# Optimization experiments

Measured on AMD Instinct MI355X. Metric: run time of the kernel, lower is better.

The kernel has to match this reference:

```python
import jax, jax.numpy as jnp
import numpy as np

FDIM, HDIM, DIM = 512, 512, 256
B, N = 64, 4096


def setup_inputs() -> dict:
    key = jax.random.key(0)
    k1, k2, k3, k4, k5 = jax.random.split(key, 5)
    image_features = jax.random.normal(k1, (B, N, FDIM), dtype=jnp.float32)
    hidden_state = jax.random.normal(k2, (B, HDIM), dtype=jnp.float32)
    # nn.Linear weights: stored [out, in]; y = x @ W.T
    W_img = jax.random.normal(k3, (DIM, FDIM), dtype=jnp.float32) * (FDIM ** -0.5)
    W_hid = jax.random.normal(k4, (DIM, HDIM), dtype=jnp.float32) * (HDIM ** -0.5)
    W_score = jax.random.normal(k5, (1, DIM), dtype=jnp.float32) * (DIM ** -0.5)
    return {"image_features": image_features, "hidden_state": hidden_state,
            "W_img": W_img, "W_hid": W_hid, "W_score": W_score}


def reference(image_features, hidden_state, W_img, W_hid, W_score):
    # proj_image: [B, N, D]
    proj_image = jnp.einsum('bnf,df->bnd', image_features, W_img)
    # proj_hidden: [B, 1, D]
    proj_hidden = jnp.einsum('bh,dh->bd', hidden_state, W_hid)[:, None, :]
    combined = jnp.tanh(proj_image + proj_hidden)            # [B, N, D]
    scores = jnp.einsum('bnd,d->bn', combined, W_score[0])   # [B, N]
    weights = jax.nn.softmax(scores, axis=-1)                # [B, N]
    context = jnp.einsum('bn,bnf->bf', weights, image_features)  # [B, F]
    return (context, weights)
```

## Files before the change

### kernel.cpp

```cpp
#include <hip/hip_runtime.h>
#include <hip/hip_bf16.h>

#define B_ 64
#define N_ 4096
#define F_ 512
#define D_ 256
#define BM 32
#define APAD 520
#define NCHUNK (N_ / BM)
#define NBLK (B_ * NCHUNK)

typedef __attribute__((ext_vector_type(8))) short short8;
typedef __attribute__((ext_vector_type(4))) float f32x4;

__device__ __forceinline__ unsigned short f2bf(float f) {
  unsigned int u = __float_as_uint(f);
  u += 0x7FFFu + ((u >> 16) & 1u);
  return (unsigned short)(u >> 16);
}

__device__ __forceinline__ unsigned int pk2bf(float x, float y) {
  float2 f; f.x = x; f.y = y;
  __hip_bfloat162 h = __float22bfloat162_rn(f);
  union { __hip_bfloat162 h2; unsigned int u; } cv; cv.h2 = h;
  return cv.u;
}

__device__ __forceinline__ float fast_tanh(float x) {
  float e = __expf(-2.0f * fabsf(x));
  float t = (1.0f - e) / (1.0f + e);
  return copysignf(t, x);
}

#define SBAR                                                                   \
  do {                                                                         \
    __builtin_amdgcn_sched_barrier(0);                                         \
    __builtin_amdgcn_s_barrier();                                              \
    __builtin_amdgcn_sched_barrier(0);                                         \
  } while (0)

#define LGKM0                                                                  \
  do {                                                                         \
    asm volatile("s_waitcnt lgkmcnt(0)" ::: "memory");                         \
    __builtin_amdgcn_sched_barrier(0);                                         \
  } while (0)

__global__ void prep_w_kernel(const float* __restrict__ Wimg,
                              unsigned short* __restrict__ wfrag) {
  int d = blockIdx.x;
  int f = threadIdx.x;
  int q = f >> 5, lg = (f >> 3) & 3, e = f & 7;
  int lr = d & 15, d16 = d >> 4;
  int lane = lg * 16 + lr;
  int idx = ((q * 16 + d16) * 64 + lane) * 8 + e;
  wfrag[idx] = f2bf(Wimg[d * F_ + f]);
}

__global__ void prep_ph_kernel(const float* __restrict__ hid,
                               const float* __restrict__ Whid,
                               float* __restrict__ ph) {
  int b = blockIdx.x, d = threadIdx.x;
  const float4* hv = (const float4*)(hid + b * F_);
  const float4* wv = (const float4*)(Whid + d * F_);
  float acc = 0.f;
#pragma unroll 4
  for (int i = 0; i < 128; i++) {
    float4 h = hv[i], w = wv[i];
    acc += h.x * w.x + h.y * w.y + h.z * w.z + h.w * w.w;
  }
  ph[b * D_ + d] = acc;
}

__global__ __launch_bounds__(256, 4) void fused_kernel(
    const float* __restrict__ feat, const unsigned short* __restrict__ wfrag,
    const float* __restrict__ ph, const float* __restrict__ wscore,
    float* __restrict__ expw, float2* __restrict__ meta,
    float* __restrict__ part) {
  __shared__ unsigned short Afull[BM * APAD];
  __shared__ float red[BM][4];
  __shared__ float sbuf[BM];
  __shared__ float ewf[BM];

  int tid = threadIdx.x;
  int lane = tid & 63, wn = tid >> 6;
  int lr = lane & 15, lg = lane >> 4;

  int blk = blockIdx.x;
  int b = blk >> 7, chunk = blk & 127;
  int n0 = chunk * BM;

  const float* arow = feat + (size_t)(b * N_ + n0) * F_;

  f32x4 acc[2][4];
#pragma unroll
  for (int m = 0; m < 2; m++)
#pragma unroll
    for (int n = 0; n < 4; n++) acc[m][n] = (f32x4)0.f;

  int r2_[4], c4_[4];
#pragma unroll
  for (int i = 0; i < 4; i++) {
    int idx4 = tid + i * 256;
    r2_[i] = idx4 >> 5;
    c4_[i] = idx4 & 31;
  }

  float4 ra0[4], ra1[4];

#define LOADA(buf, p_)                                                         \
  _Pragma("unroll") for (int i = 0; i < 4; i++)                                \
      buf[i] = *(const float4*)(arow + (size_t)r2_[i] * F_ + (p_)*128 + c4_[i] * 4);

#define CVT(buf, p_)                                                           \
  _Pragma("unroll") for (int i = 0; i < 4; i++) {                              \
    unsigned int p0 = pk2bf(buf[i].x, buf[i].y);                               \
    unsigned int p1 = pk2bf(buf[i].z, buf[i].w);                               \
    *(uint2*)(Afull + r2_[i] * APAD + (p_)*128 + c4_[i] * 4) = make_uint2(p0, p1); \
  }

  const unsigned short* bbase = wfrag + (size_t)((wn * 4) * 64 + lane) * 8;

#define QSTEP(q_)                                                              \
  {                                                                            \
    short8 bf[4];                                                              \
    _Pragma("unroll") for (int n = 0; n < 4; n++)                              \
        bf[n] = *(const short8*)(bbase + (size_t)(((q_)*16 + n) * 64) * 8);    \
    short8 a0 = *(const short8*)(Afull + lr * APAD + (q_)*32 + lg * 8);        \
    short8 a1 = *(const short8*)(Afull + (16 + lr) * APAD + (q_)*32 + lg * 8); \
    _Pragma("unroll") for (int n = 0; n < 4; n++) {                            \
      acc[0][n] = __builtin_amdgcn_mfma_f32_16x16x32_bf16(a0, bf[n], acc[0][n], 0, 0, 0); \
      acc[1][n] = __builtin_amdgcn_mfma_f32_16x16x32_bf16(a1, bf[n], acc[1][n], 0, 0, 0); \
    }                                                                          \
  }

#define PHASE(p_) { QSTEP((p_)*4+0); QSTEP((p_)*4+1); QSTEP((p_)*4+2); QSTEP((p_)*4+3); }

  LOADA(ra0, 0);
  LOADA(ra1, 1);
  CVT(ra0, 0);
  LGKM0;
  SBAR;
  LOADA(ra0, 2);
  PHASE(0);
  CVT(ra1, 1);
  LGKM0;
  SBAR;
  LOADA(ra1, 3);
  PHASE(1);
  CVT(ra0, 2);
  LGKM0;
  SBAR;
  PHASE(2);
  CVT(ra1, 3);
  LGKM0;
  SBAR;
  PHASE(3);

  float ph4[4], wv4[4];
#pragma unroll
  for (int n = 0; n < 4; n++) {
    int d = wn * 64 + n * 16 + lr;
    ph4[n] = ph[b * D_ + d];
    wv4[n] = wscore[d];
  }
#pragma unroll
  for (int m = 0; m < 2; m++) {
#pragma unroll
    for (int j = 0; j < 4; j++) {
      float p = 0.f;
#pragma unroll
      for (int n = 0; n < 4; n++)
        p += fast_tanh(acc[m][n][j] + ph4[n]) * wv4[n];
      p += __shfl_xor(p, 1);
      p += __shfl_xor(p, 2);
      p += __shfl_xor(p, 4);
      p += __shfl_xor(p, 8);
      if (lr == 0) red[m * 16 + lg * 4 + j][wn] = p;
    }
  }
  __syncthreads();
  if (tid < BM) sbuf[tid] = red[tid][0] + red[tid][1] + red[tid][2] + red[tid][3];
  __syncthreads();

  float mb = -1e30f;
#pragma unroll
  for (int r = 0; r < BM; r++) mb = fmaxf(mb, sbuf[r]);
  if (tid < BM) {
    float e = __expf(sbuf[tid] - mb);
    ewf[tid] = e;
    expw[b * N_ + n0 + tid] = e;
    float l = e;
#pragma unroll
    for (int o = 1; o < 32; o <<= 1) l += __shfl_xor(l, o);
    if (tid == 0) meta[blk] = make_float2(mb, l);
  }
  __syncthreads();

  int f0 = tid * 2;
  float a0 = 0.f, a1 = 0.f;
#pragma unroll 8
  for (int r = 0; r < BM; r++) {
    float w = ewf[r];
    unsigned int v = *(const unsigned int*)(Afull + r * APAD + f0);
    a0 += w * __uint_as_float(v << 16);
    a1 += w * __uint_as_float(v & 0xffff0000u);
  }
  float2 o; o.x = a0; o.y = a1;
  *(float2*)(part + (size_t)blk * F_ + f0) = o;
}

__global__ void finalize_kernel(const float* __restrict__ part,
                                const float2* __restrict__ meta,
                                const float* __restrict__ expw,
                                float* __restrict__ ctx,
                                float* __restrict__ wout) {
  __shared__ float sm[NCHUNK], sl[NCHUNK], se[NCHUNK];
  int b = blockIdx.x, t = threadIdx.x;
  if (t < NCHUNK) {
    float2 ml = meta[b * NCHUNK + t];
    sm[t] = ml.x;
    sl[t] = ml.y;
  }
  __syncthreads();
  float M = -1e30f;
#pragma unroll 8
  for (int i = 0; i < NCHUNK; i++) M = fmaxf(M, sm[i]);
  float Z = 0.f;
#pragma unroll 8
  for (int i = 0; i < NCHUNK; i++) Z += sl[i] * __expf(sm[i] - M);
  if (t < NCHUNK) se[t] = __expf(sm[t] - M);
  __syncthreads();
  float invZ = 1.0f / Z;
  float acc = 0.f;
#pragma unroll 8
  for (int i = 0; i < NCHUNK; i++) acc += part[(size_t)(b * NCHUNK + i) * F_ + t] * se[i];
  ctx[b * F_ + t] = acc * invZ;
#pragma unroll
  for (int k = 0; k < 8; k++) {
    int n = k * 512 + t;
    wout[b * N_ + n] = expw[b * N_ + n] * se[n >> 5] * invZ;
  }
}

extern "C" void kernel_launch(void* const* d_in, const int* in_sizes, int n_in,
                              void* d_out, int out_size, void* d_ws, size_t ws_size,
                              hipStream_t stream) {
  const float* feat   = (const float*)d_in[0];
  const float* hid    = (const float*)d_in[1];
  const float* Wimg   = (const float*)d_in[2];
  const float* Whid   = (const float*)d_in[3];
  const float* Wscore = (const float*)d_in[4];

  float* ctx  = (float*)d_out;
  float* wout = (float*)d_out + B_ * F_;

  unsigned short* wfrag = (unsigned short*)d_ws;
  float*  ph    = (float*)((char*)d_ws + 262144);
  float*  expw  = (float*)((char*)d_ws + 327680);
  float2* meta  = (float2*)((char*)d_ws + 1376256);
  float*  part  = (float*)((char*)d_ws + 1441792);

  prep_w_kernel<<<D_, F_, 0, stream>>>(Wimg, wfrag);
  prep_ph_kernel<<<B_, D_, 0, stream>>>(hid, Whid, ph);
  fused_kernel<<<NBLK, 256, 0, stream>>>(feat, wfrag, ph, Wscore, expw, meta, part);
  finalize_kernel<<<B_, 512, 0, stream>>>(part, meta, expw, ctx, wout);
}
```

Baseline: 214.2 us.

## Load whole A tile up front with row-wise coalescing, then run MFMA loop

```diff
diff --git a/kernel.cpp b/kernel.cpp
--- a/kernel.cpp
+++ b/kernel.cpp
@@ -31,19 +31,6 @@
   float t = (1.0f - e) / (1.0f + e);
   return copysignf(t, x);
 }
-
-#define SBAR                                                                   \
-  do {                                                                         \
-    __builtin_amdgcn_sched_barrier(0);                                         \
-    __builtin_amdgcn_s_barrier();                                              \
-    __builtin_amdgcn_sched_barrier(0);                                         \
-  } while (0)
-
-#define LGKM0                                                                  \
-  do {                                                                         \
-    asm volatile("s_waitcnt lgkmcnt(0)" ::: "memory");                         \
-    __builtin_amdgcn_sched_barrier(0);                                         \
-  } while (0)
 
 __global__ void prep_w_kernel(const float* __restrict__ Wimg,
                               unsigned short* __restrict__ wfrag) {
@@ -97,26 +84,33 @@
 #pragma unroll
     for (int n = 0; n < 4; n++) acc[m][n] = (f32x4)0.f;
 
-  int r2_[4], c4_[4];
-#pragma unroll
-  for (int i = 0; i < 4; i++) {
-    int idx4 = tid + i * 256;
-    r2_[i] = idx4 >> 5;
-    c4_[i] = idx4 & 31;
-  }
-
-  float4 ra0[4], ra1[4];
-
-#define LOADA(buf, p_)                                                         \
+  int rowoff_[4], c4w;
+#pragma unroll
+  for (int i = 0; i < 4; i++) rowoff_[i] = i * 2 + (tid >> 7);
+  c4w = tid & 127;
+
+  float4 ra[4], rb[4], rc[4];
+
+#define LOADR(buf, r_)                                                         \
   _Pragma("unroll") for (int i = 0; i < 4; i++)                                \
-      buf[i] = *(const float4*)(arow + (size_t)r2_[i] * F_ + (p_)*128 + c4_[i] * 4);
-
-#define CVT(buf, p_)                                                           \
+      buf[i] = *(const float4*)(arow + (size_t)((r_)*8 + rowoff_[i]) * F_ + c4w * 4);
+
+#define CVTR(buf, r_)                                                          \
   _Pragma("unroll") for (int i = 0; i < 4; i++) {                              \
     unsigned int p0 = pk2bf(buf[i].x, buf[i].y);                               \
     unsigned int p1 = pk2bf(buf[i].z, buf[i].w);                               \
-    *(uint2*)(Afull + r2_[i] * APAD + (p_)*128 + c4_[i] * 4) = make_uint2(p0, p1); \
-  }
+    *(uint2*)(Afull + ((r_)*8 + rowoff_[i]) * APAD + c4w * 4) = make_uint2(p0, p1); \
+  }
+
+  LOADR(ra, 0);
+  LOADR(rb, 1);
+  LOADR(rc, 2);
+  CVTR(ra, 0);
+  LOADR(ra, 3);
+  CVTR(rb, 1);
+  CVTR(rc, 2);
+  CVTR(ra, 3);
+  __syncthreads();
 
   const unsigned short* bbase = wfrag + (size_t)((wn * 4) * 64 + lane) * 8;
 
@@ -133,28 +127,10 @@
     }                                                                          \
   }
 
-#define PHASE(p_) { QSTEP((p_)*4+0); QSTEP((p_)*4+1); QSTEP((p_)*4+2); QSTEP((p_)*4+3); }
-
-  LOADA(ra0, 0);
-  LOADA(ra1, 1);
-  CVT(ra0, 0);
-  LGKM0;
-  SBAR;
-  LOADA(ra0, 2);
-  PHASE(0);
-  CVT(ra1, 1);
-  LGKM0;
-  SBAR;
-  LOADA(ra1, 3);
-  PHASE(1);
-  CVT(ra0, 2);
-  LGKM0;
-  SBAR;
-  PHASE(2);
-  CVT(ra1, 3);
-  LGKM0;
-  SBAR;
-  PHASE(3);
+  __builtin_amdgcn_s_setprio(1);
+#pragma unroll
+  for (int q = 0; q < 16; q++) { QSTEP(q); }
+  __builtin_amdgcn_s_setprio(0);
 
   float ph4[4], wv4[4];
 #pragma unroll
```

Result: slower. 230.3 us (+7.5%).

## Make fused kernel persistent over 16 row tiles with DMA-staged weight fragments

Applied to the files above, without the earlier changes.

```diff
diff --git a/kernel.cpp b/kernel.cpp
--- a/kernel.cpp
+++ b/kernel.cpp
@@ -5,10 +5,11 @@
 #define N_ 4096
 #define F_ 512
 #define D_ 256
-#define BM 32
+#define BM 64
 #define APAD 520
 #define NCHUNK (N_ / BM)
-#define NBLK (B_ * NCHUNK)
+#define GT 16
+#define NBLK (B_ * NCHUNK / GT)
 
 typedef __attribute__((ext_vector_type(8))) short short8;
 typedef __attribute__((ext_vector_type(4))) float f32x4;
@@ -42,6 +43,12 @@
 #define LGKM0                                                                  \
   do {                                                                         \
     asm volatile("s_waitcnt lgkmcnt(0)" ::: "memory");                         \
+    __builtin_amdgcn_sched_barrier(0);                                         \
+  } while (0)
+
+#define VMC4                                                                   \
+  do {                                                                         \
+    asm volatile("s_waitcnt vmcnt(4)" ::: "memory");                           \
     __builtin_amdgcn_sched_barrier(0);                                         \
   } while (0)
 
@@ -71,12 +78,13 @@
   ph[b * D_ + d] = acc;
 }
 
-__global__ __launch_bounds__(256, 4) void fused_kernel(
+__global__ __launch_bounds__(256, 1) void fused_kernel(
     const float* __restrict__ feat, const unsigned short* __restrict__ wfrag,
     const float* __restrict__ ph, const float* __restrict__ wscore,
     float* __restrict__ expw, float2* __restrict__ meta,
     float* __restrict__ part) {
   __shared__ unsigned short Afull[BM * APAD];
+  __shared__ unsigned short Bst[2][16384];
   __shared__ float red[BM][4];
   __shared__ float sbuf[BM];
   __shared__ float ewf[BM];
@@ -86,127 +94,135 @@
   int lr = lane & 15, lg = lane >> 4;
 
   int blk = blockIdx.x;
-  int b = blk >> 7, chunk = blk & 127;
-  int n0 = chunk * BM;
-
-  const float* arow = feat + (size_t)(b * N_ + n0) * F_;
-
-  f32x4 acc[2][4];
-#pragma unroll
-  for (int m = 0; m < 2; m++)
-#pragma unroll
-    for (int n = 0; n < 4; n++) acc[m][n] = (f32x4)0.f;
-
-  int r2_[4], c4_[4];
-#pragma unroll
-  for (int i = 0; i < 4; i++) {
-    int idx4 = tid + i * 256;
-    r2_[i] = idx4 >> 5;
-    c4_[i] = idx4 & 31;
-  }
-
-  float4 ra0[4], ra1[4];
-
-#define LOADA(buf, p_)                                                         \
+  int b = blk >> 2, j = blk & 3;
+
+  float ph4[4], ws4[4];
+#pragma unroll
+  for (int n = 0; n < 4; n++) {
+    int d = wn * 64 + n * 16 + lr;
+    ph4[n] = ph[b * D_ + d];
+    ws4[n] = wscore[d];
+  }
+
+  int r_ = tid >> 2, c16 = (tid & 3) * 16;
+  const float* arow = feat + ((size_t)b * N_ + (size_t)j * GT * BM) * F_;
+
+  float4 rs0_[4], rs1_[4];
+
+#define LOADS(buf, ptr, kt_)                                                   \
   _Pragma("unroll") for (int i = 0; i < 4; i++)                                \
-      buf[i] = *(const float4*)(arow + (size_t)r2_[i] * F_ + (p_)*128 + c4_[i] * 4);
-
-#define CVT(buf, p_)                                                           \
+      buf[i] = *(const float4*)((ptr) + (size_t)r_ * F_ + (kt_)*64 + c16 + i * 4);
+
+#define CVT(buf, kt_)                                                          \
   _Pragma("unroll") for (int i = 0; i < 4; i++) {                              \
     unsigned int p0 = pk2bf(buf[i].x, buf[i].y);                               \
     unsigned int p1 = pk2bf(buf[i].z, buf[i].w);                               \
-    *(uint2*)(Afull + r2_[i] * APAD + (p_)*128 + c4_[i] * 4) = make_uint2(p0, p1); \
-  }
-
-  const unsigned short* bbase = wfrag + (size_t)((wn * 4) * 64 + lane) * 8;
-
-#define QSTEP(q_)                                                              \
+    *(uint2*)(Afull + r_ * APAD + (kt_)*64 + c16 + i * 4) = make_uint2(p0, p1);\
+  }
+
+#define DMAB(bs, kt_)                                                          \
+  do {                                                                         \
+    __builtin_amdgcn_sched_barrier(0);                                         \
+    _Pragma("unroll") for (int i = 0; i < 8; i++) {                            \
+      int fg = wn * 8 + i;                                                     \
+      const char* gsrc = (const char*)wfrag + ((size_t)(kt_)*32 + fg) * 1024 + lane * 16; \
+      char* ldst = (char*)&Bst[bs][0] + fg * 1024 + lane * 16;                 \
+      __builtin_amdgcn_global_load_lds(                                        \
+          (const __attribute__((address_space(1))) void*)gsrc,                 \
+          (__attribute__((address_space(3))) void*)ldst, 16, 0, 0);            \
+    }                                                                          \
+    __builtin_amdgcn_sched_barrier(0);                                         \
+  } while (0)
+
+#define QSTEP(kt_, ql_, bs)                                                    \
   {                                                                            \
-    short8 bf[4];                                                              \
+    short8 bf[4], af[4];                                                       \
     _Pragma("unroll") for (int n = 0; n < 4; n++)                              \
-        bf[n] = *(const short8*)(bbase + (size_t)(((q_)*16 + n) * 64) * 8);    \
-    short8 a0 = *(const short8*)(Afull + lr * APAD + (q_)*32 + lg * 8);        \
-    short8 a1 = *(const short8*)(Afull + (16 + lr) * APAD + (q_)*32 + lg * 8); \
-    _Pragma("unroll") for (int n = 0; n < 4; n++) {                            \
-      acc[0][n] = __builtin_amdgcn_mfma_f32_16x16x32_bf16(a0, bf[n], acc[0][n], 0, 0, 0); \
-      acc[1][n] = __builtin_amdgcn_mfma_f32_16x16x32_bf16(a1, bf[n], acc[1][n], 0, 0, 0); \
-    }                                                                          \
-  }
-
-#define PHASE(p_) { QSTEP((p_)*4+0); QSTEP((p_)*4+1); QSTEP((p_)*4+2); QSTEP((p_)*4+3); }
-
-  LOADA(ra0, 0);
-  LOADA(ra1, 1);
-  CVT(ra0, 0);
-  LGKM0;
-  SBAR;
-  LOADA(ra0, 2);
-  PHASE(0);
-  CVT(ra1, 1);
-  LGKM0;
-  SBAR;
-  LOADA(ra1, 3);
-  PHASE(1);
-  CVT(ra0, 2);
-  LGKM0;
-  SBAR;
-  PHASE(2);
-  CVT(ra1, 3);
-  LGKM0;
-  SBAR;
-  PHASE(3);
-
-  float ph4[4], wv4[4];
-#pragma unroll
-  for (int n = 0; n < 4; n++) {
-    int d = wn * 64 + n * 16 + lr;
-    ph4[n] = ph[b * D_ + d];
-    wv4[n] = wscore[d];
-  }
-#pragma unroll
-  for (int m = 0; m < 2; m++) {
-#pragma unroll
-    for (int j = 0; j < 4; j++) {
-      float p = 0.f;
-#pragma unroll
-      for (int n = 0; n < 4; n++)
-        p += fast_tanh(acc[m][n][j] + ph4[n]) * wv4[n];
-      p += __shfl_xor(p, 1);
-      p += __shfl_xor(p, 2);
-      p += __shfl_xor(p, 4);
-      p += __shfl_xor(p, 8);
-      if (lr == 0) red[m * 16 + lg * 4 + j][wn] = p;
+        bf[n] = *(const short8*)(&Bst[bs][(((ql_)*16 + wn * 4 + n) * 64 + lane) * 8]); \
+    _Pragma("unroll") for (int m = 0; m < 4; m++)                              \
+        af[m] = *(const short8*)(Afull + (m * 16 + lr) * APAD + (kt_)*64 + (ql_)*32 + lg * 8); \
+    _Pragma("unroll") for (int m = 0; m < 4; m++)                              \
+      _Pragma("unroll") for (int n = 0; n < 4; n++)                            \
+        acc[m][n] = __builtin_amdgcn_mfma_f32_16x16x32_bf16(af[m], bf[n], acc[m][n], 0, 0, 0); \
+  }
+
+#define COMPUTE(kt_, bs) { QSTEP(kt_, 0, bs); QSTEP(kt_, 1, bs); }
+
+  DMAB(0, 0);
+  LOADS(rs0_, arow, 0);
+  LOADS(rs1_, arow, 1);
+
+#pragma unroll 1
+  for (int t = 0; t < GT; t++) {
+    const float* nrow = (t < GT - 1) ? (arow + (size_t)BM * F_) : arow;
+    f32x4 acc[4][4];
+#pragma unroll
+    for (int m = 0; m < 4; m++)
+#pragma unroll
+      for (int n = 0; n < 4; n++) acc[m][n] = (f32x4)0.f;
+
+    CVT(rs0_, 0); LGKM0; VMC4; SBAR;
+    DMAB(1, 1); LOADS(rs0_, arow, 2); COMPUTE(0, 0); CVT(rs1_, 1); LGKM0; VMC4; SBAR;
+    DMAB(0, 2); LOADS(rs1_, arow, 3); COMPUTE(1, 1); CVT(rs0_, 2); LGKM0; VMC4; SBAR;
+    DMAB(1, 3); LOADS(rs0_, arow, 4); COMPUTE(2, 0); CVT(rs1_, 3); LGKM0; VMC4; SBAR;
+    DMAB(0, 4); LOADS(rs1_, arow, 5); COMPUTE(3, 1); CVT(rs0_, 4); LGKM0; VMC4; SBAR;
+    DMAB(1, 5); LOADS(rs0_, arow, 6); COMPUTE(4, 0); CVT(rs1_, 5); LGKM0; VMC4; SBAR;
+    DMAB(0, 6); LOADS(rs1_, arow, 7); COMPUTE(5, 1); CVT(rs0_, 6); LGKM0; VMC4; SBAR;
+    DMAB(1, 7); LOADS(rs0_, nrow, 0); COMPUTE(6, 0); CVT(rs1_, 7); LGKM0; VMC4; SBAR;
+    DMAB(0, 8); LOADS(rs1_, nrow, 1); COMPUTE(7, 1); SBAR;
+
+#pragma unroll
+    for (int m = 0; m < 4; m++) {
+#pragma unroll
+      for (int jj = 0; jj < 4; jj++) {
+        float p = 0.f;
+#pragma unroll
+        for (int n = 0; n < 4; n++)
+          p += fast_tanh(acc[m][n][jj] + ph4[n]) * ws4[n];
+        p += __shfl_xor(p, 1);
+        p += __shfl_xor(p, 2);
+        p += __shfl_xor(p, 4);
+        p += __shfl_xor(p, 8);
+        if (lr == 0) red[m * 16 + lg * 4 + jj][wn] = p;
+      }
     }
-  }
-  __syncthreads();
-  if (tid < BM) sbuf[tid] = red[tid][0] + red[tid][1] + red[tid][2] + red[tid][3];
-  __syncthreads();
-
-  float mb = -1e30f;
-#pragma unroll
-  for (int r = 0; r < BM; r++) mb = fmaxf(mb, sbuf[r]);
-  if (tid < BM) {
-    float e = __expf(sbuf[tid] - mb);
-    ewf[tid] = e;
-    expw[b * N_ + n0 + tid] = e;
-    float l = e;
-#pragma unroll
-    for (int o = 1; o < 32; o <<= 1) l += __shfl_xor(l, o);
-    if (tid == 0) meta[blk] = make_float2(mb, l);
-  }
-  __syncthreads();
-
-  int f0 = tid * 2;
-  float a0 = 0.f, a1 = 0.f;
-#pragma unroll 8
-  for (int r = 0; r < BM; r++) {
-    float w = ewf[r];
-    unsigned int v = *(const unsigned int*)(Afull + r * APAD + f0);
-    a0 += w * __uint_as_float(v << 16);
-    a1 += w * __uint_as_float(v & 0xffff0000u);
-  }
-  float2 o; o.x = a0; o.y = a1;
-  *(float2*)(part + (size_t)blk * F_ + f0) = o;
+    LGKM0; SBAR;
+    if (tid < BM) sbuf[tid] = red[tid][0] + red[tid][1] + red[tid][2] + red[tid][3];
+    LGKM0; SBAR;
+
+    int tile = j * GT + t;
+    int n0 = tile * BM;
+    float mb = -1e30f;
+#pragma unroll
+    for (int r = 0; r < BM; r++) mb = fmaxf(mb, sbuf[r]);
+    if (tid < BM) {
+      float e = __expf(sbuf[tid] - mb);
+      ewf[tid] = e;
+      expw[b * N_ + n0 + tid] = e;
+      float l = e;
+#pragma unroll
+      for (int o = 1; o < 64; o <<= 1) l += __shfl_xor(l, o);
+      if (tid == 0) meta[b * NCHUNK + tile] = make_float2(mb, l);
+    }
+    LGKM0; SBAR;
+
+    {
+      int f0 = tid * 2;
+      float a0 = 0.f, a1 = 0.f;
+#pragma unroll 8
+      for (int r = 0; r < BM; r++) {
+        float w = ewf[r];
+        unsigned int v = *(const unsigned int*)(Afull + r * APAD + f0);
+        a0 += w * __uint_as_float(v << 16);
+        a1 += w * __uint_as_float(v & 0xffff0000u);
+      }
+      float2 o; o.x = a0; o.y = a1;
+      *(float2*)(part + (size_t)(b * NCHUNK + tile) * F_ + f0) = o;
+    }
+    SBAR;
+
+    arow = nrow;
+  }
 }
 
 __global__ void finalize_kernel(const float* __restrict__ part,
@@ -238,7 +254,7 @@
 #pragma unroll
   for (int k = 0; k < 8; k++) {
     int n = k * 512 + t;
-    wout[b * N_ + n] = expw[b * N_ + n] * se[n >> 5] * invZ;
+    wout[b * N_ + n] = expw[b * N_ + n] * se[n >> 6] * invZ;
   }
 }
 
@@ -255,12 +271,13 @@
   float* wout = (float*)d_out + B_ * F_;
 
   unsigned short* wfrag = (unsigned short*)d_ws;
-  float*  ph    = (float*)((char*)d_ws + 262144);
-  float*  expw  = (float*)((char*)d_ws + 327680);
-  float2* meta  = (float2*)((char*)d_ws + 1376256);
-  float*  part  = (float*)((char*)d_ws + 1441792);
+  float*  ph    = (float*)((char*)d_ws + 524288);
+  float*  expw  = (float*)((char*)d_ws + 589824);
+  float2* meta  = (float2*)((char*)d_ws + 1638400);
+  float*  part  = (float*)((char*)d_ws + 1671168);
 
   prep_w_kernel<<<D_, F_, 0, stream>>>(Wimg, wfrag);
+  hipMemcpyAsync((char*)d_ws + 262144, d_ws, 262144, hipMemcpyDeviceToDevice, stream);
   prep_ph_kernel<<<B_, D_, 0, stream>>>(hid, Whid, ph);
   fused_kernel<<<NBLK, 256, 0, stream>>>(feat, wfrag, ph, Wscore, expw, meta, part);
   finalize_kernel<<<B_, 512, 0, stream>>>(part, meta, expw, ctx, wout);
```

New measurement: 337.0 us. +57.3%, slower.
